# Optimization experiments

Hardware: AMD Instinct MI355X
Metric: run time of the kernel (lower is better)

## Reference

```python
import jax, jax.numpy as jnp
import numpy as np

N, F_IN, H, F_OUT = 8192, 256, 128, 16
POOL_RATIO = 0.5


def setup_inputs() -> dict:
    key = jax.random.key(0)
    ks = jax.random.split(key, 12)
    # Sparse-ish symmetric adjacency with zero diagonal (avg degree ~32).
    A = (jax.random.uniform(ks[0], (N, N)) < (32.0 / N)).astype(jnp.float32)
    A = jnp.maximum(A, A.T) * (1.0 - jnp.eye(N, dtype=jnp.float32))
    x = jax.random.normal(ks[1], (N, F_IN), dtype=jnp.float32)

    def lin(k, fin, fout):
        return (jax.random.normal(k, (fin, fout), dtype=jnp.float32) / np.float32(np.sqrt(fin)))

    return {
        "x": x, "A": A,
        "W0": lin(ks[2], F_IN, H), "b0": jnp.zeros((H,), jnp.float32),
        "W1": lin(ks[3], H, H),    "b1": jnp.zeros((H,), jnp.float32),
        "pw": lin(ks[4], H, 1),    "pb": jnp.zeros((1,), jnp.float32),
        "Wu": lin(ks[5], H, H),    "bu": jnp.zeros((H,), jnp.float32),
        "Wf": lin(ks[6], H, F_OUT), "bf": jnp.zeros((F_OUT,), jnp.float32),
    }


def _norm_adj(A):
    # normalize(): add self-loops (diag of A is 0), row-normalize D^-1 (A+I)
    Ah = A + jnp.eye(A.shape[0], dtype=A.dtype)
    r = jnp.sum(Ah, axis=1)
    r_inv = jnp.where(r > 0, 1.0 / r, 0.0)
    return Ah * r_inv[:, None]


def _gconv(x, A, W, b, act):
    h = x @ W + b          # nn.Linear
    h = _norm_adj(A) @ h   # spmm with row-normalized adjacency
    return act(h)


def reference(x, A, W0, b0, W1, b1, pw, pb, Wu, bu, Wf, bf):
    relu = jax.nn.relu
    ident = lambda t: t
    # down gconv 0
    h0 = _gconv(x, A, W0, b0, relu)                       # [N, H]
    # gPool: score -> l2-normalize -> sigmoid -> top-k gather
    score = h0 @ pw + pb                                  # [N, 1]
    score = score / jnp.sqrt(jnp.sum(score ** 2))
    score = jax.nn.sigmoid(score[:, 0])                   # [N]
    k = max(2, int(POOL_RATIO * h0.shape[0]))
    vals, idx = jax.lax.top_k(score, k)                   # [k]
    xp = h0[idx] * vals[:, None]                          # gated gather [k, H]
    Ap = A[idx][:, idx]                                   # pooled adjacency [k, k]
    # down gconv 1 (bottleneck, no pool after)
    h1 = _gconv(xp, Ap, W1, b1, relu)                     # [k, H]
    # gUnpool: zero-scatter back to N nodes
    xu = jnp.zeros((A.shape[0], h1.shape[1]), h1.dtype).at[idx].set(h1)
    # up gconv
    hu = _gconv(xu, A, Wu, bu, relu)                      # [N, H]
    # final gconv (identity activation) + log_softmax
    hf = _gconv(hu, A, Wf, bf, ident)                     # [N, F_OUT]
    return jax.nn.log_softmax(hf, axis=1)
```

## Files before the change

kernel.cpp:

```cpp
#include <hip/hip_runtime.h>
#include <math.h>

#define N_NODES 8192
#define FIN 256
#define HDIM 128
#define FOUTD 16
#define KSEL 4096
#define CAP 128

typedef unsigned int uint;
typedef unsigned short ushort;

static __device__ __forceinline__ ushort f2bf(float f) {
    uint u = __float_as_uint(f);
    return (ushort)((u + 0x7FFFu + ((u >> 16) & 1u)) >> 16);
}
static __device__ __forceinline__ float bf_lo(uint u) { return __uint_as_float(u << 16); }
static __device__ __forceinline__ float bf_hi(uint u) { return __uint_as_float(u & 0xFFFF0000u); }

__global__ __launch_bounds__(256) void csru_gemm0(const float* __restrict__ A,
                                                  int* __restrict__ cols,
                                                  int* __restrict__ degU,
                                                  int* __restrict__ degT,
                                                  const float* __restrict__ x,
                                                  const float* __restrict__ W0,
                                                  const float* __restrict__ b0,
                                                  float* __restrict__ T0) {
    int grp = blockIdx.x / 17;
    int rem = blockIdx.x - grp * 17;
    if (rem < 16) {
        int i = grp * 16 + rem;
        __shared__ int cnt;
        __shared__ int scols[CAP];
        if (threadIdx.x == 0) cnt = 0;
        __syncthreads();
        const float4* Arow = (const float4*)(A + (size_t)i * N_NODES);
        for (int c4 = (i >> 2) + threadIdx.x; c4 < N_NODES / 4; c4 += 256) {
            float4 v = Arow[c4];
            int base = c4 * 4;
            if (v.x != 0.0f && base + 0 > i) { int p = atomicAdd(&cnt, 1); if (p < CAP) scols[p] = base; }
            if (v.y != 0.0f && base + 1 > i) { int p = atomicAdd(&cnt, 1); if (p < CAP) scols[p] = base + 1; }
            if (v.z != 0.0f && base + 2 > i) { int p = atomicAdd(&cnt, 1); if (p < CAP) scols[p] = base + 2; }
            if (v.w != 0.0f && base + 3 > i) { int p = atomicAdd(&cnt, 1); if (p < CAP) scols[p] = base + 3; }
        }
        __syncthreads();
        int c = cnt; if (c > CAP) c = CAP;
        for (int t = threadIdx.x; t < c; t += 256)
            cols[(size_t)i * CAP + t] = scols[t];
        if (threadIdx.x == 0) { degU[i] = c; degT[i] = c; }
    } else {
        int half = threadIdx.x >> 7;
        int tid = threadIdx.x & 127;
        int row0 = grp * 16 + half * 8;
        float acc[8];
#pragma unroll
        for (int r = 0; r < 8; r++) acc[r] = 0.0f;
        const float* Xb = x + (size_t)row0 * FIN;
        for (int k = 0; k < FIN; k += 4) {
            float w0 = W0[(k + 0) * HDIM + tid];
            float w1 = W0[(k + 1) * HDIM + tid];
            float w2 = W0[(k + 2) * HDIM + tid];
            float w3 = W0[(k + 3) * HDIM + tid];
#pragma unroll
            for (int r = 0; r < 8; r++) {
                const float* xr = Xb + r * FIN + k;
                acc[r] = fmaf(xr[0], w0, acc[r]);
                acc[r] = fmaf(xr[1], w1, acc[r]);
                acc[r] = fmaf(xr[2], w2, acc[r]);
                acc[r] = fmaf(xr[3], w3, acc[r]);
            }
        }
        float bias = b0[tid];
#pragma unroll
        for (int r = 0; r < 8; r++)
            T0[(size_t)(row0 + r) * HDIM + tid] = acc[r] + bias;
    }
}

__global__ __launch_bounds__(256) void csr_mirror(int* __restrict__ cols,
                                                  const int* __restrict__ degU,
                                                  int* __restrict__ degT) {
    int wv = threadIdx.x >> 6, lane = threadIdx.x & 63;
    int i = blockIdx.x * 4 + wv;
    int du = degU[i];
    for (int t = lane; t < du; t += 64) {
        int j = cols[(size_t)i * CAP + t];
        int pos = atomicAdd(&degT[j], 1);
        if (pos < CAP) cols[(size_t)j * CAP + pos] = i;
    }
}

__global__ __launch_bounds__(128) void spmm_score_p1(const float* __restrict__ T0,
                                                     const int* __restrict__ cols,
                                                     const int* __restrict__ degT,
                                                     const float* __restrict__ pw,
                                                     const float* __restrict__ pb,
                                                     const float* __restrict__ W1,
                                                     uint* __restrict__ P1u,
                                                     float* __restrict__ sraw) {
    int wv = threadIdx.x >> 6, lane = threadIdx.x & 63;
    int row = blockIdx.x * 2 + wv;
    const float2* T2p = (const float2*)T0;
    const int* cl = cols + (size_t)row * CAP;
    int d = degT[row]; if (d > CAP) d = CAP;
    float2 a0 = {0.f, 0.f}, a1 = {0.f, 0.f}, a2 = {0.f, 0.f}, a3 = {0.f, 0.f};
    int j = 0;
    for (; j + 4 <= d; j += 4) {
        int c0 = cl[j], c1 = cl[j + 1], c2 = cl[j + 2], c3 = cl[j + 3];
        float2 v0 = T2p[(size_t)c0 * 64 + lane];
        float2 v1 = T2p[(size_t)c1 * 64 + lane];
        float2 v2 = T2p[(size_t)c2 * 64 + lane];
        float2 v3 = T2p[(size_t)c3 * 64 + lane];
        a0.x += v0.x; a0.y += v0.y;
        a1.x += v1.x; a1.y += v1.y;
        a2.x += v2.x; a2.y += v2.y;
        a3.x += v3.x; a3.y += v3.y;
    }
    for (; j < d; j++) {
        float2 v0 = T2p[(size_t)cl[j] * 64 + lane];
        a0.x += v0.x; a0.y += v0.y;
    }
    float2 own = T2p[(size_t)row * 64 + lane];
    float inv = 1.0f / (float)(1 + d);
    float hx = fmaxf((own.x + (a0.x + a1.x) + (a2.x + a3.x)) * inv, 0.f);
    float hy = fmaxf((own.y + (a0.y + a1.y) + (a2.y + a3.y)) * inv, 0.f);
    float2 pw2 = ((const float2*)pw)[lane];
    float v = hx * pw2.x + hy * pw2.y;
    for (int off = 32; off; off >>= 1) v += __shfl_down(v, off);
    if (lane == 0) sraw[row] = v + pb[0];
    float accx = 0.f, accy = 0.f;
    const float2* W1r = (const float2*)W1;
#pragma unroll 4
    for (int kk = 0; kk < 64; kk++) {
        float xk0 = __uint_as_float(__builtin_amdgcn_readlane(__float_as_uint(hx), kk));
        float xk1 = __uint_as_float(__builtin_amdgcn_readlane(__float_as_uint(hy), kk));
        float2 w0 = W1r[(size_t)(2 * kk) * 64 + lane];
        float2 w1 = W1r[(size_t)(2 * kk + 1) * 64 + lane];
        accx = fmaf(xk0, w0.x, accx); accy = fmaf(xk0, w0.y, accy);
        accx = fmaf(xk1, w1.x, accx); accy = fmaf(xk1, w1.y, accy);
    }
    P1u[(size_t)row * 64 + lane] = (uint)f2bf(accx) | ((uint)f2bf(accy) << 16);
}

__global__ __launch_bounds__(256) void topk_radix(const float* __restrict__ sraw,
                                                  int* __restrict__ sel,
                                                  float* __restrict__ g) {
    int tid = threadIdx.x;
    int lane = tid & 63, wv = tid >> 6;
    float v[32];
    unsigned key[32];
    float ss = 0.f;
#pragma unroll
    for (int e = 0; e < 32; e++) {
        float x = sraw[tid * 32 + e];
        v[e] = x; ss += x * x;
        unsigned b = __float_as_uint(x);
        key[e] = (b & 0x80000000u) ? ~b : (b | 0x80000000u);
    }
    __shared__ float fr[4];
    for (int off = 32; off; off >>= 1) ss += __shfl_down(ss, off);
    if (lane == 0) fr[wv] = ss;
    __syncthreads();
    float inv_norm = 1.0f / sqrtf(fr[0] + fr[1] + fr[2] + fr[3]);

    __shared__ int hist[256];
    __shared__ int wred[4];
    __shared__ int bd, bkneed;
    unsigned prefix = 0; int kneed = KSEL;
    for (int pass = 0; pass < 4; pass++) {
        int shift = 24 - 8 * pass;
        unsigned maskAbove = (pass == 0) ? 0u : (0xFFFFFFFFu << (shift + 8));
        hist[tid] = 0;
        __syncthreads();
#pragma unroll
        for (int e = 0; e < 32; e++)
            if ((key[e] & maskAbove) == prefix)
                atomicAdd(&hist[(key[e] >> shift) & 255], 1);
        __syncthreads();
        int h = hist[tid];
        int s = h;
#pragma unroll
        for (int off = 1; off < 64; off <<= 1) {
            int t = __shfl_down(s, off);
            if (lane + off < 64) s += t;
        }
        if (lane == 0) wred[wv] = s;
        __syncthreads();
        int addhi = 0;
        for (int w = wv + 1; w < 4; w++) addhi += wred[w];
        int s_here = s + addhi;
        int s_next = s_here - h;
        if (s_here >= kneed && s_next < kneed) { bd = tid; bkneed = kneed - s_next; }
        __syncthreads();
        prefix |= ((unsigned)bd) << shift;
        kneed = bkneed;
        __syncthreads();
    }
    unsigned T = prefix;
    int eq = 0;
#pragma unroll
    for (int e = 0; e < 32; e++) eq += (key[e] == T);
    int p = eq;
#pragma unroll
    for (int off = 1; off < 64; off <<= 1) {
        int t = __shfl_up(p, off);
        if (lane >= off) p += t;
    }
    __shared__ int wpre[4];
    if (lane == 63) wpre[wv] = p;
    __syncthreads();
    int base = 0;
    for (int w = 0; w < wv; w++) base += wpre[w];
    int excl = base + p - eq;
    int seen = 0;
#pragma unroll
    for (int e = 0; e < 32; e++) {
        int i = tid * 32 + e;
        int s2;
        if (key[e] > T) s2 = 1;
        else if (key[e] == T) { s2 = (excl + seen < kneed) ? 1 : 0; seen++; }
        else s2 = 0;
        sel[i] = s2;
        g[i] = s2 ? (1.0f / (1.0f + expf(-(v[e] * inv_norm)))) : 0.0f;
    }
}

__global__ __launch_bounds__(64) void pool_gemm(const uint* __restrict__ P1u,
                                                const int* __restrict__ cols,
                                                const int* __restrict__ degT,
                                                const int* __restrict__ sel,
                                                const float* __restrict__ g,
                                                const float* __restrict__ b1,
                                                const float* __restrict__ Wu,
                                                const float* __restrict__ bu,
                                                uint* __restrict__ T2u) {
    int row = blockIdx.x;
    int t = threadIdx.x;
    float2 biasU = ((const float2*)bu)[t];
    if (!sel[row]) {
        T2u[(size_t)row * 64 + t] = (uint)f2bf(biasU.x) | ((uint)f2bf(biasU.y) << 16);
        return;
    }
    const int* cl = cols + (size_t)row * CAP;
    int d = degT[row]; if (d > CAP) d = CAP;
    uint su = P1u[(size_t)row * 64 + t];
    float grow = g[row];
    float ax = bf_lo(su) * grow, ay = bf_hi(su) * grow;
    int cnt = 0;
    for (int j = 0; j < d; j++) {
        int c = cl[j];
        if (sel[c]) {
            cnt++;
            uint u = P1u[(size_t)c * 64 + t];
            float gc = g[c];
            ax = fmaf(bf_lo(u), gc, ax); ay = fmaf(bf_hi(u), gc, ay);
        }
    }
    float2 b1p = ((const float2*)b1)[t];
    float inv = 1.0f / (float)(1 + cnt);
    float xux = fmaxf(fmaf(ax, inv, b1p.x), 0.f);
    float xuy = fmaxf(fmaf(ay, inv, b1p.y), 0.f);
    float accx = biasU.x, accy = biasU.y;
    const float2* Wur = (const float2*)Wu;
#pragma unroll 4
    for (int kk = 0; kk < 64; kk++) {
        float xk0 = __uint_as_float(__builtin_amdgcn_readlane(__float_as_uint(xux), kk));
        float xk1 = __uint_as_float(__builtin_amdgcn_readlane(__float_as_uint(xuy), kk));
        float2 w0 = Wur[(size_t)(2 * kk) * 64 + t];
        float2 w1 = Wur[(size_t)(2 * kk + 1) * 64 + t];
        accx = fmaf(xk0, w0.x, accx); accy = fmaf(xk0, w0.y, accy);
        accx = fmaf(xk1, w1.x, accx); accy = fmaf(xk1, w1.y, accy);
    }
    T2u[(size_t)row * 64 + t] = (uint)f2bf(accx) | ((uint)f2bf(accy) << 16);
}

__global__ __launch_bounds__(64) void up_gemm16(const uint* __restrict__ T2u,
                                                const int* __restrict__ cols,
                                                const int* __restrict__ degT,
                                                const float* __restrict__ Wf,
                                                const float* __restrict__ bf_,
                                                float* __restrict__ T3) {
    int row = blockIdx.x;
    int t = threadIdx.x;
    const int* cl = cols + (size_t)row * CAP;
    int d = degT[row]; if (d > CAP) d = CAP;
    uint su = T2u[(size_t)row * 64 + t];
    float ax = bf_lo(su), ay = bf_hi(su);
    for (int j = 0; j < d; j++) {
        uint u = T2u[(size_t)cl[j] * 64 + t];
        ax += bf_lo(u); ay += bf_hi(u);
    }
    float inv = 1.0f / (float)(1 + d);
    float hux = fmaxf(ax * inv, 0.f);
    float huy = fmaxf(ay * inv, 0.f);
    __shared__ float hs[128];
    hs[2 * t] = hux; hs[2 * t + 1] = huy;
    __syncthreads();
    int c = t & 15, gg = t >> 4;
    float p = 0.f;
#pragma unroll 8
    for (int kk = 0; kk < 32; kk++) {
        int k = gg * 32 + kk;
        p = fmaf(hs[k], Wf[k * FOUTD + c], p);
    }
    p += __shfl_xor(p, 16);
    p += __shfl_xor(p, 32);
    if (t < 16) T3[(size_t)row * FOUTD + t] = p + bf_[t];
}

__global__ __launch_bounds__(64) void spmm16_lsm(const float* __restrict__ T3,
                                                 const int* __restrict__ cols,
                                                 const int* __restrict__ degT,
                                                 float* __restrict__ out) {
    int lane = threadIdx.x;
    int r = lane >> 4, c = lane & 15;
    int row = blockIdx.x * 4 + r;
    const int* cl = cols + (size_t)row * CAP;
    int d = degT[row]; if (d > CAP) d = CAP;
    float acc = T3[(size_t)row * FOUTD + c];
    for (int j = 0; j < d; j++) acc += T3[(size_t)cl[j] * FOUTD + c];
    float v = acc / (float)(1 + d);
    float m = v;
    for (int off = 1; off < 16; off <<= 1) m = fmaxf(m, __shfl_xor(m, off, 16));
    float e = expf(v - m);
    float s = e;
    for (int off = 1; off < 16; off <<= 1) s += __shfl_xor(s, off, 16);
    out[(size_t)row * FOUTD + c] = v - m - logf(s);
}

extern "C" void kernel_launch(void* const* d_in, const int* in_sizes, int n_in,
                              void* d_out, int out_size, void* d_ws, size_t ws_size,
                              hipStream_t stream) {
    const float* x  = (const float*)d_in[0];
    const float* A  = (const float*)d_in[1];
    const float* W0 = (const float*)d_in[2];
    const float* b0 = (const float*)d_in[3];
    const float* W1 = (const float*)d_in[4];
    const float* b1 = (const float*)d_in[5];
    const float* pw = (const float*)d_in[6];
    const float* pb = (const float*)d_in[7];
    const float* Wu = (const float*)d_in[8];
    const float* bu = (const float*)d_in[9];
    const float* Wf = (const float*)d_in[10];
    const float* bf = (const float*)d_in[11];
    float* out = (float*)d_out;

    char* ws = (char*)d_ws;
    const size_t MB = 1024 * 1024;
    int*   cols = (int*)  (ws);
    int*   degU = (int*)  (ws + 4 * MB);
    int*   degT = (int*)  (ws + 4 * MB + 65536);
    float* T0   = (float*)(ws + 5  * MB);
    uint*  P1   = (uint*) (ws + 9  * MB);
    uint*  T2   = (uint*) (ws + 11 * MB);
    float* T3   = (float*)(ws + 13 * MB);
    float* sraw = (float*)(ws + 14 * MB);
    int*   sel  = (int*)  (ws + 14 * MB + 65536);
    float* g    = (float*)(ws + 14 * MB + 131072);

    csru_gemm0<<<512 * 17, 256, 0, stream>>>(A, cols, degU, degT, x, W0, b0, T0);
    csr_mirror<<<N_NODES / 4, 256, 0, stream>>>(cols, degU, degT);
    spmm_score_p1<<<N_NODES / 2, 128, 0, stream>>>(T0, cols, degT, pw, pb, W1, P1, sraw);
    topk_radix<<<1, 256, 0, stream>>>(sraw, sel, g);
    pool_gemm<<<N_NODES, 64, 0, stream>>>(P1, cols, degT, sel, g, b1, Wu, bu, T2);
    up_gemm16<<<N_NODES, 64, 0, stream>>>(T2, cols, degT, Wf, bf, T3);
    spmm16_lsm<<<N_NODES / 4, 64, 0, stream>>>(T3, cols, degT, out);
}
```

Baseline: 596.5 us.

## Fuse CSR mirroring into the adjacency scan and balance triangular row pairs

```diff
diff --git a/kernel.cpp b/kernel.cpp
--- a/kernel.cpp
+++ b/kernel.cpp
@@ -18,36 +18,58 @@
 static __device__ __forceinline__ float bf_lo(uint u) { return __uint_as_float(u << 16); }
 static __device__ __forceinline__ float bf_hi(uint u) { return __uint_as_float(u & 0xFFFF0000u); }
 
-__global__ __launch_bounds__(256) void csru_gemm0(const float* __restrict__ A,
+__global__ __launch_bounds__(256) void csrp_gemm0(const float* __restrict__ A,
                                                   int* __restrict__ cols,
+                                                  int* __restrict__ cols2,
                                                   int* __restrict__ degU,
-                                                  int* __restrict__ degT,
+                                                  int* __restrict__ cnt2,
                                                   const float* __restrict__ x,
                                                   const float* __restrict__ W0,
                                                   const float* __restrict__ b0,
                                                   float* __restrict__ T0) {
-    int grp = blockIdx.x / 17;
-    int rem = blockIdx.x - grp * 17;
-    if (rem < 16) {
-        int i = grp * 16 + rem;
-        __shared__ int cnt;
-        __shared__ int scols[CAP];
-        if (threadIdx.x == 0) cnt = 0;
-        __syncthreads();
-        const float4* Arow = (const float4*)(A + (size_t)i * N_NODES);
-        for (int c4 = (i >> 2) + threadIdx.x; c4 < N_NODES / 4; c4 += 256) {
-            float4 v = Arow[c4];
+    int grp = blockIdx.x / 9;
+    int rem = blockIdx.x - grp * 9;
+    if (rem < 8) {
+        int p  = grp * 8 + rem;
+        int ra = p, rb = N_NODES - 1 - p;
+        __shared__ int cA, cB;
+        __shared__ int sA[CAP], sB[CAP];
+        if (threadIdx.x == 0) { cA = 0; cB = 0; }
+        __syncthreads();
+        const float4* Ar = (const float4*)(A + (size_t)ra * N_NODES);
+        for (int c4 = (ra >> 2) + threadIdx.x; c4 < N_NODES / 4; c4 += 256) {
+            float4 v = Ar[c4];
             int base = c4 * 4;
-            if (v.x != 0.0f && base + 0 > i) { int p = atomicAdd(&cnt, 1); if (p < CAP) scols[p] = base; }
-            if (v.y != 0.0f && base + 1 > i) { int p = atomicAdd(&cnt, 1); if (p < CAP) scols[p] = base + 1; }
-            if (v.z != 0.0f && base + 2 > i) { int p = atomicAdd(&cnt, 1); if (p < CAP) scols[p] = base + 2; }
-            if (v.w != 0.0f && base + 3 > i) { int p = atomicAdd(&cnt, 1); if (p < CAP) scols[p] = base + 3; }
-        }
-        __syncthreads();
-        int c = cnt; if (c > CAP) c = CAP;
-        for (int t = threadIdx.x; t < c; t += 256)
-            cols[(size_t)i * CAP + t] = scols[t];
-        if (threadIdx.x == 0) { degU[i] = c; degT[i] = c; }
+            if (v.x != 0.0f && base + 0 > ra) { int q = atomicAdd(&cA, 1); if (q < CAP) sA[q] = base; }
+            if (v.y != 0.0f && base + 1 > ra) { int q = atomicAdd(&cA, 1); if (q < CAP) sA[q] = base + 1; }
+            if (v.z != 0.0f && base + 2 > ra) { int q = atomicAdd(&cA, 1); if (q < CAP) sA[q] = base + 2; }
+            if (v.w != 0.0f && base + 3 > ra) { int q = atomicAdd(&cA, 1); if (q < CAP) sA[q] = base + 3; }
+        }
+        const float4* Br = (const float4*)(A + (size_t)rb * N_NODES);
+        for (int c4 = (rb >> 2) + threadIdx.x; c4 < N_NODES / 4; c4 += 256) {
+            float4 v = Br[c4];
+            int base = c4 * 4;
+            if (v.x != 0.0f && base + 0 > rb) { int q = atomicAdd(&cB, 1); if (q < CAP) sB[q] = base; }
+            if (v.y != 0.0f && base + 1 > rb) { int q = atomicAdd(&cB, 1); if (q < CAP) sB[q] = base + 1; }
+            if (v.z != 0.0f && base + 2 > rb) { int q = atomicAdd(&cB, 1); if (q < CAP) sB[q] = base + 2; }
+            if (v.w != 0.0f && base + 3 > rb) { int q = atomicAdd(&cB, 1); if (q < CAP) sB[q] = base + 3; }
+        }
+        __syncthreads();
+        int dA = cA; if (dA > CAP) dA = CAP;
+        int dB = cB; if (dB > CAP) dB = CAP;
+        for (int t = threadIdx.x; t < dA; t += 256) {
+            int j = sA[t];
+            cols[(size_t)ra * CAP + t] = j;
+            int pos = atomicAdd(&cnt2[j], 1);
+            if (pos < CAP) cols2[(size_t)j * CAP + pos] = ra;
+        }
+        for (int t = threadIdx.x; t < dB; t += 256) {
+            int j = sB[t];
+            cols[(size_t)rb * CAP + t] = j;
+            int pos = atomicAdd(&cnt2[j], 1);
+            if (pos < CAP) cols2[(size_t)j * CAP + pos] = rb;
+        }
+        if (threadIdx.x == 0) { degU[ra] = dA; degU[rb] = dB; }
     } else {
         int half = threadIdx.x >> 7;
         int tid = threadIdx.x & 127;
@@ -77,22 +99,11 @@
     }
 }
 
-__global__ __launch_bounds__(256) void csr_mirror(int* __restrict__ cols,
-                                                  const int* __restrict__ degU,
-                                                  int* __restrict__ degT) {
-    int wv = threadIdx.x >> 6, lane = threadIdx.x & 63;
-    int i = blockIdx.x * 4 + wv;
-    int du = degU[i];
-    for (int t = lane; t < du; t += 64) {
-        int j = cols[(size_t)i * CAP + t];
-        int pos = atomicAdd(&degT[j], 1);
-        if (pos < CAP) cols[(size_t)j * CAP + pos] = i;
-    }
-}
-
 __global__ __launch_bounds__(128) void spmm_score_p1(const float* __restrict__ T0,
                                                      const int* __restrict__ cols,
-                                                     const int* __restrict__ degT,
+                                                     const int* __restrict__ cols2,
+                                                     const int* __restrict__ degU,
+                                                     const int* __restrict__ cnt2,
                                                      const float* __restrict__ pw,
                                                      const float* __restrict__ pb,
                                                      const float* __restrict__ W1,
@@ -101,25 +112,30 @@
     int wv = threadIdx.x >> 6, lane = threadIdx.x & 63;
     int row = blockIdx.x * 2 + wv;
     const float2* T2p = (const float2*)T0;
-    const int* cl = cols + (size_t)row * CAP;
-    int d = degT[row]; if (d > CAP) d = CAP;
+    int dU = degU[row]; if (dU > CAP) dU = CAP;
+    int dM = cnt2[row]; if (dM > CAP) dM = CAP;
     float2 a0 = {0.f, 0.f}, a1 = {0.f, 0.f}, a2 = {0.f, 0.f}, a3 = {0.f, 0.f};
-    int j = 0;
-    for (; j + 4 <= d; j += 4) {
-        int c0 = cl[j], c1 = cl[j + 1], c2 = cl[j + 2], c3 = cl[j + 3];
-        float2 v0 = T2p[(size_t)c0 * 64 + lane];
-        float2 v1 = T2p[(size_t)c1 * 64 + lane];
-        float2 v2 = T2p[(size_t)c2 * 64 + lane];
-        float2 v3 = T2p[(size_t)c3 * 64 + lane];
-        a0.x += v0.x; a0.y += v0.y;
-        a1.x += v1.x; a1.y += v1.y;
-        a2.x += v2.x; a2.y += v2.y;
-        a3.x += v3.x; a3.y += v3.y;
-    }
-    for (; j < d; j++) {
-        float2 v0 = T2p[(size_t)cl[j] * 64 + lane];
-        a0.x += v0.x; a0.y += v0.y;
-    }
+    for (int part = 0; part < 2; part++) {
+        const int* cl = (part ? cols2 : cols) + (size_t)row * CAP;
+        int d = part ? dM : dU;
+        int j = 0;
+        for (; j + 4 <= d; j += 4) {
+            int c0 = cl[j], c1 = cl[j + 1], c2 = cl[j + 2], c3 = cl[j + 3];
+            float2 v0 = T2p[(size_t)c0 * 64 + lane];
+            float2 v1 = T2p[(size_t)c1 * 64 + lane];
+            float2 v2 = T2p[(size_t)c2 * 64 + lane];
+            float2 v3 = T2p[(size_t)c3 * 64 + lane];
+            a0.x += v0.x; a0.y += v0.y;
+            a1.x += v1.x; a1.y += v1.y;
+            a2.x += v2.x; a2.y += v2.y;
+            a3.x += v3.x; a3.y += v3.y;
+        }
+        for (; j < d; j++) {
+            float2 v0 = T2p[(size_t)cl[j] * 64 + lane];
+            a0.x += v0.x; a0.y += v0.y;
+        }
+    }
+    int d = dU + dM;
     float2 own = T2p[(size_t)row * 64 + lane];
     float inv = 1.0f / (float)(1 + d);
     float hx = fmaxf((own.x + (a0.x + a1.x) + (a2.x + a3.x)) * inv, 0.f);
@@ -227,7 +243,9 @@
 
 __global__ __launch_bounds__(64) void pool_gemm(const uint* __restrict__ P1u,
                                                 const int* __restrict__ cols,
-                                                const int* __restrict__ degT,
+                                                const int* __restrict__ cols2,
+                                                const int* __restrict__ degU,
+                                                const int* __restrict__ cnt2,
                                                 const int* __restrict__ sel,
                                                 const float* __restrict__ g,
                                                 const float* __restrict__ b1,
@@ -241,19 +259,23 @@
         T2u[(size_t)row * 64 + t] = (uint)f2bf(biasU.x) | ((uint)f2bf(biasU.y) << 16);
         return;
     }
-    const int* cl = cols + (size_t)row * CAP;
-    int d = degT[row]; if (d > CAP) d = CAP;
     uint su = P1u[(size_t)row * 64 + t];
     float grow = g[row];
     float ax = bf_lo(su) * grow, ay = bf_hi(su) * grow;
     int cnt = 0;
-    for (int j = 0; j < d; j++) {
-        int c = cl[j];
-        if (sel[c]) {
-            cnt++;
-            uint u = P1u[(size_t)c * 64 + t];
-            float gc = g[c];
-            ax = fmaf(bf_lo(u), gc, ax); ay = fmaf(bf_hi(u), gc, ay);
+    int dU = degU[row]; if (dU > CAP) dU = CAP;
+    int dM = cnt2[row]; if (dM > CAP) dM = CAP;
+    for (int part = 0; part < 2; part++) {
+        const int* cl = (part ? cols2 : cols) + (size_t)row * CAP;
+        int d = part ? dM : dU;
+        for (int j = 0; j < d; j++) {
+            int c = cl[j];
+            if (sel[c]) {
+                cnt++;
+                uint u = P1u[(size_t)c * 64 + t];
+                float gc = g[c];
+                ax = fmaf(bf_lo(u), gc, ax); ay = fmaf(bf_hi(u), gc, ay);
+            }
         }
     }
     float2 b1p = ((const float2*)b1)[t];
@@ -276,20 +298,27 @@
 
 __global__ __launch_bounds__(64) void up_gemm16(const uint* __restrict__ T2u,
                                                 const int* __restrict__ cols,
-                                                const int* __restrict__ degT,
+                                                const int* __restrict__ cols2,
+                                                const int* __restrict__ degU,
+                                                const int* __restrict__ cnt2,
                                                 const float* __restrict__ Wf,
                                                 const float* __restrict__ bf_,
                                                 float* __restrict__ T3) {
     int row = blockIdx.x;
     int t = threadIdx.x;
-    const int* cl = cols + (size_t)row * CAP;
-    int d = degT[row]; if (d > CAP) d = CAP;
     uint su = T2u[(size_t)row * 64 + t];
     float ax = bf_lo(su), ay = bf_hi(su);
-    for (int j = 0; j < d; j++) {
-        uint u = T2u[(size_t)cl[j] * 64 + t];
-        ax += bf_lo(u); ay += bf_hi(u);
-    }
+    int dU = degU[row]; if (dU > CAP) dU = CAP;
+    int dM = cnt2[row]; if (dM > CAP) dM = CAP;
+    for (int part = 0; part < 2; part++) {
+        const int* cl = (part ? cols2 : cols) + (size_t)row * CAP;
+        int d = part ? dM : dU;
+        for (int j = 0; j < d; j++) {
+            uint u = T2u[(size_t)cl[j] * 64 + t];
+            ax += bf_lo(u); ay += bf_hi(u);
+        }
+    }
+    int d = dU + dM;
     float inv = 1.0f / (float)(1 + d);
     float hux = fmaxf(ax * inv, 0.f);
     float huy = fmaxf(ay * inv, 0.f);
@@ -310,15 +339,22 @@
 
 __global__ __launch_bounds__(64) void spmm16_lsm(const float* __restrict__ T3,
                                                  const int* __restrict__ cols,
-                                                 const int* __restrict__ degT,
+                                                 const int* __restrict__ cols2,
+                                                 const int* __restrict__ degU,
+                                                 const int* __restrict__ cnt2,
                                                  float* __restrict__ out) {
     int lane = threadIdx.x;
     int r = lane >> 4, c = lane & 15;
     int row = blockIdx.x * 4 + r;
-    const int* cl = cols + (size_t)row * CAP;
-    int d = degT[row]; if (d > CAP) d = CAP;
     float acc = T3[(size_t)row * FOUTD + c];
-    for (int j = 0; j < d; j++) acc += T3[(size_t)cl[j] * FOUTD + c];
+    int dU = degU[row]; if (dU > CAP) dU = CAP;
+    int dM = cnt2[row]; if (dM > CAP) dM = CAP;
+    for (int part = 0; part < 2; part++) {
+        const int* cl = (part ? cols2 : cols) + (size_t)row * CAP;
+        int d = part ? dM : dU;
+        for (int j = 0; j < d; j++) acc += T3[(size_t)cl[j] * FOUTD + c];
+    }
+    int d = dU + dM;
     float v = acc / (float)(1 + d);
     float m = v;
     for (int off = 1; off < 16; off <<= 1) m = fmaxf(m, __shfl_xor(m, off, 16));
@@ -347,22 +383,25 @@
 
     char* ws = (char*)d_ws;
     const size_t MB = 1024 * 1024;
-    int*   cols = (int*)  (ws);
-    int*   degU = (int*)  (ws + 4 * MB);
-    int*   degT = (int*)  (ws + 4 * MB + 65536);
-    float* T0   = (float*)(ws + 5  * MB);
-    uint*  P1   = (uint*) (ws + 9  * MB);
-    uint*  T2   = (uint*) (ws + 11 * MB);
-    float* T3   = (float*)(ws + 13 * MB);
-    float* sraw = (float*)(ws + 14 * MB);
-    int*   sel  = (int*)  (ws + 14 * MB + 65536);
-    float* g    = (float*)(ws + 14 * MB + 131072);
-
-    csru_gemm0<<<512 * 17, 256, 0, stream>>>(A, cols, degU, degT, x, W0, b0, T0);
-    csr_mirror<<<N_NODES / 4, 256, 0, stream>>>(cols, degU, degT);
-    spmm_score_p1<<<N_NODES / 2, 128, 0, stream>>>(T0, cols, degT, pw, pb, W1, P1, sraw);
+    int*   cols  = (int*)  (ws);
+    int*   cols2 = (int*)  (ws + 4 * MB);
+    int*   degU  = (int*)  (ws + 8 * MB);
+    int*   cnt2  = (int*)  (ws + 8 * MB + 65536);
+    float* T0    = (float*)(ws + 9  * MB);
+    uint*  P1    = (uint*) (ws + 13 * MB);
+    uint*  T2    = (uint*) (ws + 15 * MB);
+    float* T3    = (float*)(ws + 17 * MB);
+    float* sraw  = (float*)(ws + 18 * MB);
+    int*   sel   = (int*)  (ws + 18 * MB + 65536);
+    float* g     = (float*)(ws + 18 * MB + 131072);
+
+    hipMemsetAsync(cnt2, 0, N_NODES * sizeof(int), stream);
+    csrp_gemm0<<<512 * 9, 256, 0, stream>>>(A, cols, cols2, degU, cnt2, x, W0, b0, T0);
+    spmm_score_p1<<<N_NODES / 2, 128, 0, stream>>>(T0, cols, cols2, degU, cnt2,
+                                                   pw, pb, W1, P1, sraw);
     topk_radix<<<1, 256, 0, stream>>>(sraw, sel, g);
-    pool_gemm<<<N_NODES, 64, 0, stream>>>(P1, cols, degT, sel, g, b1, Wu, bu, T2);
-    up_gemm16<<<N_NODES, 64, 0, stream>>>(T2, cols, degT, Wf, bf, T3);
-    spmm16_lsm<<<N_NODES / 4, 64, 0, stream>>>(T3, cols, degT, out);
-}
+    pool_gemm<<<N_NODES, 64, 0, stream>>>(P1, cols, cols2, degU, cnt2, sel, g,
+                                          b1, Wu, bu, T2);
+    up_gemm16<<<N_NODES, 64, 0, stream>>>(T2, cols, cols2, degU, cnt2, Wf, bf, T3);
+    spmm16_lsm<<<N_NODES / 4, 64, 0, stream>>>(T3, cols, cols2, degU, cnt2, out);
+}
```

Result: faster. 583.4 us (-2.2%).
